# Performance work log

Measured on AMD Instinct MI355X. Metric: run time of the kernel, lower is better.

The kernel has to match this reference:

```python
import jax, jax.numpy as jnp
import numpy as np

N_NODES = 100000


def gcn_conv(x, src, dst, W, b, n_nodes):
    """PyG GCNConv: add self-loops, symmetric deg^-1/2 normalization,
    linear transform, scatter-add aggregation, bias."""
    loop = jnp.arange(n_nodes, dtype=src.dtype)
    s = jnp.concatenate([src, loop])
    d = jnp.concatenate([dst, loop])
    # degree of destination nodes (includes self-loops)
    deg = jax.ops.segment_sum(jnp.ones(s.shape[0], dtype=x.dtype), d,
                              num_segments=n_nodes)
    dis = jnp.where(deg > 0, jax.lax.rsqrt(deg), 0.0)  # deg^-1/2
    norm = dis[s] * dis[d]                              # [E+N]
    h = x @ W                                           # [N, out]
    msg = h[s] * norm[:, None]                          # gather + scale
    out = jax.ops.segment_sum(msg, d, num_segments=n_nodes)  # scatter-add
    return out + b


def setup_inputs() -> dict:
    key = jax.random.key(0)
    k1, k2, k3, k4 = jax.random.split(key, 4)
    F_in, H, C = 500, 64, 10
    x = jax.random.normal(k1, (N_NODES, F_in), dtype=jnp.float32)
    edge_index = jax.random.randint(k2, (2, 1600000), 0, N_NODES,
                                    dtype=jnp.int32)
    W1 = jax.random.normal(k3, (F_in, H), dtype=jnp.float32) / np.sqrt(F_in)
    b1 = jnp.zeros((H,), dtype=jnp.float32)
    W2 = jax.random.normal(k4, (H, C), dtype=jnp.float32) / np.sqrt(H)
    b2 = jnp.zeros((C,), dtype=jnp.float32)
    return {"x": x, "edge_index": edge_index,
            "W1": W1, "b1": b1, "W2": W2, "b2": b2}


def reference(x, edge_index, W1, b1, W2, b2):
    src, dst = edge_index[0], edge_index[1]
    h = gcn_conv(x, src, dst, W1, b1, N_NODES)
    h = jax.nn.relu(h)
    # dropout is identity at inference (training=False)
    out = gcn_conv(h, src, dst, W2, b2, N_NODES)
    return out
```

## Files before the change

### kernel.cpp

```cpp
#include <hip/hip_runtime.h>

#define F_IN 500
#define HDIM 64
#define CDIM 10
#define KPAD 512
#define NSTAGE 16
#define H2LD 16

typedef __attribute__((ext_vector_type(8))) short bf16x8;
typedef __attribute__((ext_vector_type(4))) float floatx4;

__device__ inline unsigned short f2bf(float f) {
    unsigned int u = __float_as_uint(f);
    u += 0x7fffu + ((u >> 16) & 1u);
    return (unsigned short)(u >> 16);
}
__device__ inline float bflo(unsigned int u) { return __uint_as_float(u << 16); }
__device__ inline float bfhi(unsigned int u) { return __uint_as_float(u & 0xffff0000u); }

__device__ inline void split8(float4 a, float4 b, bf16x8& xh, bf16x8& xl) {
    float xv[8] = {a.x, a.y, a.z, a.w, b.x, b.y, b.z, b.w};
#pragma unroll
    for (int j = 0; j < 8; ++j) {
        unsigned int u = __float_as_uint(xv[j]);
        xh[j] = (short)(u >> 16);
        float r = xv[j] - __uint_as_float(u & 0xffff0000u);
        xl[j] = (short)(__float_as_uint(r) >> 16);
    }
}

__global__ __launch_bounds__(256) void prep_kernel(
        const int* __restrict__ dst, int E, int* __restrict__ deg,
        int* __restrict__ erank,
        const float* __restrict__ W1, unsigned short* __restrict__ whf,
        unsigned short* __restrict__ wlf, int degB) {
    int bid = blockIdx.x;
    if (bid < degB) {
        int e = bid * 256 + threadIdx.x;
        if (e < E) erank[e] = atomicAdd(&deg[dst[e]], 1);
    } else {
        int idx = (bid - degB) * 256 + threadIdx.x;
        if (idx >= KPAD * HDIM) return;
        int k = idx >> 6;
        int f = idx & 63;
        float w = (k < F_IN) ? W1[k * HDIM + f] : 0.f;
        unsigned int b = __float_as_uint(w);
        unsigned short hh = (unsigned short)(b >> 16);
        float wl = w - __uint_as_float(b & 0xffff0000u);
        unsigned short ll = (unsigned short)(__float_as_uint(wl) >> 16);
        int kb = k >> 5, q = (k >> 3) & 3, j = k & 7;
        int fb = f >> 4, fl = f & 15;
        int lane = (q << 4) | fl;
        size_t o = ((((size_t)kb * 4 + fb) * 64 + lane) << 3) | (size_t)j;
        whf[o] = hh;
        wlf[o] = ll;
    }
}

__global__ void scan_block_kernel(const int* __restrict__ deg,
                                  int* __restrict__ row_ptr,
                                  int* __restrict__ blk_sum,
                                  float* __restrict__ dis, int Np1) {
    __shared__ int wsum[16];
    int i = blockIdx.x * 1024 + threadIdx.x;
    int v = (i < Np1 - 1) ? deg[i] : 0;
    if (i < Np1 - 1) dis[i] = rsqrtf((float)(v + 1));
    int lane = threadIdx.x & 63;
    int wid = threadIdx.x >> 6;
    int x = v;
#pragma unroll
    for (int off = 1; off < 64; off <<= 1) {
        int y = __shfl_up(x, off);
        if (lane >= off) x += y;
    }
    if (lane == 63) wsum[wid] = x;
    __syncthreads();
    if (threadIdx.x < 16) {
        int ws = wsum[threadIdx.x];
#pragma unroll
        for (int off = 1; off < 16; off <<= 1) {
            int y = __shfl_up(ws, off);
            if ((int)threadIdx.x >= off) ws += y;
        }
        wsum[threadIdx.x] = ws;
    }
    __syncthreads();
    int wp = (wid > 0) ? wsum[wid - 1] : 0;
    if (i < Np1) row_ptr[i] = wp + x - v;
    if (threadIdx.x == 1023) blk_sum[blockIdx.x] = wp + x;
}

__global__ void scan_top_kernel(int* __restrict__ blk_sum, int nb) {
    int carry = 0;
    for (int base = 0; base < nb; base += 64) {
        int i = base + (int)threadIdx.x;
        int v = (i < nb) ? blk_sum[i] : 0;
        int x = v;
#pragma unroll
        for (int off = 1; off < 64; off <<= 1) {
            int y = __shfl_up(x, off);
            if ((int)threadIdx.x >= off) x += y;
        }
        if (i < nb) blk_sum[i] = carry + x - v;
        carry += __shfl(x, 63);
    }
}

__global__ __launch_bounds__(256) void csr_gemm_kernel(
        const float* __restrict__ x, const unsigned short* __restrict__ whf,
        const unsigned short* __restrict__ wlf, const float* __restrict__ dis,
        unsigned short* __restrict__ h1b, int N,
        const int* __restrict__ src, const int* __restrict__ dst,
        const int* __restrict__ erank,
        const int* __restrict__ row_ptr, const int* __restrict__ blk_sum,
        int* __restrict__ csr_src, int E,
        int gemmB) {
    const int bid = blockIdx.x;
    const int g5 = bid / 5;
    const bool isGemm = (bid % 5 == 0) && (g5 < gemmB);
    if (!isGemm) {
        int before = (bid + 4) / 5;
        if (before > gemmB) before = gemmB;
        int cb = bid - before;
        int e = cb * 256 + threadIdx.x;
        if (e >= E) return;
        int d = dst[e];
        csr_src[row_ptr[d] + blk_sum[d >> 10] + erank[e]] = src[e];
        return;
    }
    const int lane = threadIdx.x & 63;
    const int wid = (g5 << 2) + (threadIdx.x >> 6);
    const int n0 = wid * 16;
    if (n0 >= N) return;
    const int q = lane >> 4;
    const int fl = lane & 15;
    const float* xp = x + (size_t)(n0 + fl) * F_IN + q * 8;

    const bf16x8* whv = (const bf16x8*)whf;
    const bf16x8* wlv = (const bf16x8*)wlf;

    floatx4 acc[4];
#pragma unroll
    for (int fb = 0; fb < 4; ++fb) acc[fb] = (floatx4){0.f, 0.f, 0.f, 0.f};

    float4 xa[4], xb[4];
    bf16x8 wh[2][4], wl[2][4];

    xa[0] = *(const float4*)(xp);
    xb[0] = *(const float4*)(xp + 4);
    xa[1] = *(const float4*)(xp + 32);
    xb[1] = *(const float4*)(xp + 36);
    xa[2] = *(const float4*)(xp + 64);
    xb[2] = *(const float4*)(xp + 68);
#pragma unroll
    for (int fb = 0; fb < 4; ++fb) {
        wh[0][fb] = whv[(size_t)fb * 64 + lane];
        wl[0][fb] = wlv[(size_t)fb * 64 + lane];
    }

#pragma unroll
    for (int kb = 0; kb < NSTAGE - 1; ++kb) {
        const int cw = kb & 1, nw = cw ^ 1;
#pragma unroll
        for (int fb = 0; fb < 4; ++fb) {
            wh[nw][fb] = whv[(size_t)((kb + 1) * 4 + fb) * 64 + lane];
            wl[nw][fb] = wlv[(size_t)((kb + 1) * 4 + fb) * 64 + lane];
        }
        if (kb + 3 < NSTAGE - 1) {
            xa[(kb + 3) & 3] = *(const float4*)(xp + (kb + 3) * 32);
            xb[(kb + 3) & 3] = *(const float4*)(xp + (kb + 3) * 32 + 4);
        }
        bf16x8 xh, xl;
        split8(xa[kb & 3], xb[kb & 3], xh, xl);
#pragma unroll
        for (int fb = 0; fb < 4; ++fb) {
            acc[fb] = __builtin_amdgcn_mfma_f32_16x16x32_bf16(xh, wh[cw][fb], acc[fb], 0, 0, 0);
            acc[fb] = __builtin_amdgcn_mfma_f32_16x16x32_bf16(xl, wh[cw][fb], acc[fb], 0, 0, 0);
            acc[fb] = __builtin_amdgcn_mfma_f32_16x16x32_bf16(xh, wl[cw][fb], acc[fb], 0, 0, 0);
        }
    }
    {
        const int kb = NSTAGE - 1;
        float xv[8];
#pragma unroll
        for (int j = 0; j < 8; ++j) {
            int kk = kb * 32 + q * 8 + j;
            xv[j] = (kk < F_IN) ? xp[kb * 32 + j] : 0.f;
        }
        bf16x8 xh, xl;
#pragma unroll
        for (int j = 0; j < 8; ++j) {
            unsigned int u = __float_as_uint(xv[j]);
            xh[j] = (short)(u >> 16);
            float r = xv[j] - __uint_as_float(u & 0xffff0000u);
            xl[j] = (short)(__float_as_uint(r) >> 16);
        }
        const int cw = kb & 1;
#pragma unroll
        for (int fb = 0; fb < 4; ++fb) {
            acc[fb] = __builtin_amdgcn_mfma_f32_16x16x32_bf16(xh, wh[cw][fb], acc[fb], 0, 0, 0);
            acc[fb] = __builtin_amdgcn_mfma_f32_16x16x32_bf16(xl, wh[cw][fb], acc[fb], 0, 0, 0);
            acc[fb] = __builtin_amdgcn_mfma_f32_16x16x32_bf16(xh, wl[cw][fb], acc[fb], 0, 0, 0);
        }
    }
#pragma unroll
    for (int r = 0; r < 4; ++r) {
        int node = n0 + q * 4 + r;
        float dn = dis[node];
#pragma unroll
        for (int fb = 0; fb < 4; ++fb) {
            h1b[(size_t)node * HDIM + fb * 16 + fl] = f2bf(acc[fb][r] * dn);
        }
    }
}

__global__ __launch_bounds__(256) void gather1_l2_kernel(
        const int* __restrict__ row_ptr, const int* __restrict__ blk_sum,
        const int* __restrict__ csr_src, const float* __restrict__ dis,
        const unsigned short* __restrict__ h1b,
        const float* __restrict__ b1, const float* __restrict__ W2,
        float* __restrict__ h2s, int N) {
    __shared__ float sW2[HDIM * CDIM];
    __shared__ float sB1[HDIM];
    for (int i = threadIdx.x; i < HDIM * CDIM; i += 256) sW2[i] = W2[i];
    if (threadIdx.x < HDIM) sB1[threadIdx.x] = b1[threadIdx.x];
    __syncthreads();
    int nid = blockIdx.x * 4 + (threadIdx.x >> 6);
    if (nid >= N) return;
    int node = __builtin_amdgcn_readfirstlane(nid);
    int lane = threadIdx.x & 63;
    int half = lane >> 5;
    int c = lane & 31;
    int beg = row_ptr[node] + blk_sum[node >> 10];
    int end = row_ptr[node + 1] + blk_sum[(node + 1) >> 10];
    float dd = dis[node];
    float a0 = 0.f, a1 = 0.f;
    if (half == 0) {
        unsigned int w = *reinterpret_cast<const unsigned int*>(
            h1b + (size_t)node * HDIM + 2 * c);
        a0 = bflo(w);
        a1 = bfhi(w);
    }
    int p = beg + half;
    for (; p + 14 < end; p += 16) {
        unsigned int wv[8];
#pragma unroll
        for (int i = 0; i < 8; ++i) {
            int s = csr_src[p + 2 * i];
            wv[i] = *reinterpret_cast<const unsigned int*>(
                h1b + (size_t)s * HDIM + 2 * c);
        }
#pragma unroll
        for (int i = 0; i < 8; ++i) {
            a0 += bflo(wv[i]);
            a1 += bfhi(wv[i]);
        }
    }
    for (; p < end; p += 2) {
        int s0 = csr_src[p];
        unsigned int w0 = *reinterpret_cast<const unsigned int*>(
            h1b + (size_t)s0 * HDIM + 2 * c);
        a0 += bflo(w0);
        a1 += bfhi(w0);
    }
    a0 += __shfl_xor(a0, 32);
    a1 += __shfl_xor(a1, 32);
    float t0 = a0 * dd + sB1[2 * c];
    float t1 = a1 * dd + sB1[2 * c + 1];
    t0 = t0 > 0.f ? t0 : 0.f;
    t1 = t1 > 0.f ? t1 : 0.f;
    float pj[CDIM];
#pragma unroll
    for (int j = 0; j < CDIM; ++j)
        pj[j] = t0 * sW2[(2 * c) * CDIM + j] + t1 * sW2[(2 * c + 1) * CDIM + j];
#pragma unroll
    for (int off = 1; off < 32; off <<= 1) {
#pragma unroll
        for (int j = 0; j < CDIM; ++j) pj[j] += __shfl_xor(pj[j], off);
    }
    if (lane < CDIM) {
        float v = pj[0];
#pragma unroll
        for (int j = 1; j < CDIM; ++j)
            if (lane == j) v = pj[j];
        h2s[(size_t)node * H2LD + lane] = v * dd;
    }
}

__global__ __launch_bounds__(256) void gather2_kernel(
        const int* __restrict__ row_ptr, const int* __restrict__ blk_sum,
        const int* __restrict__ csr_src, const float* __restrict__ dis,
        const float* __restrict__ h2s, const float* __restrict__ b2,
        float* __restrict__ out, int N) {
    int nid = blockIdx.x * 4 + (threadIdx.x >> 6);
    if (nid >= N) return;
    int node = __builtin_amdgcn_readfirstlane(nid);
    int lane = threadIdx.x & 63;
    int g = lane >> 4;
    int j = lane & 15;
    int beg = row_ptr[node] + blk_sum[node >> 10];
    int end = row_ptr[node + 1] + blk_sum[(node + 1) >> 10];
    float acc = 0.f;
    int p = beg + g;
    for (; p + 12 < end; p += 16) {
        int s0 = csr_src[p];
        int s1 = csr_src[p + 4];
        int s2 = csr_src[p + 8];
        int s3 = csr_src[p + 12];
        float v0 = (j < CDIM) ? h2s[(size_t)s0 * H2LD + j] : 0.f;
        float v1 = (j < CDIM) ? h2s[(size_t)s1 * H2LD + j] : 0.f;
        float v2 = (j < CDIM) ? h2s[(size_t)s2 * H2LD + j] : 0.f;
        float v3 = (j < CDIM) ? h2s[(size_t)s3 * H2LD + j] : 0.f;
        acc += (v0 + v1) + (v2 + v3);
    }
    for (; p < end; p += 4) {
        int s0 = csr_src[p];
        acc += (j < CDIM) ? h2s[(size_t)s0 * H2LD + j] : 0.f;
    }
    acc += __shfl_xor(acc, 16);
    acc += __shfl_xor(acc, 32);
    if (lane < CDIM) {
        float dd = dis[node];
        out[(size_t)node * CDIM + lane] =
            b2[lane] + dd * (acc + h2s[(size_t)node * H2LD + lane]);
    }
}

static inline char* align256(char* p) {
    return (char*)(((uintptr_t)p + 255) & ~(uintptr_t)255);
}

extern "C" void kernel_launch(void* const* d_in, const int* in_sizes, int n_in,
                              void* d_out, int out_size, void* d_ws,
                              size_t ws_size, hipStream_t stream) {
    const float* x  = (const float*)d_in[0];
    const int*   ei = (const int*)d_in[1];
    const float* W1 = (const float*)d_in[2];
    const float* b1 = (const float*)d_in[3];
    const float* W2 = (const float*)d_in[4];
    const float* b2 = (const float*)d_in[5];

    const int N = in_sizes[0] / F_IN;
    const int E = in_sizes[1] / 2;
    const int* src = ei;
    const int* dst = ei + E;
    float* out = (float*)d_out;

    const int Np1 = N + 1;
    const int nscan_blocks = (Np1 + 1023) / 1024;

    char* w = (char*)d_ws;
    int* deg = (int*)w;                  w = align256(w + (size_t)N * 4);
    char* zero_end = w;
    int* erank = (int*)w;                w = align256(w + (size_t)E * 4);
    float* dis = (float*)w;              w = align256(w + (size_t)N * 4);
    int* row_ptr = (int*)w;              w = align256(w + (size_t)(N + 4) * 4);
    int* blk_sum = (int*)w;              w = align256(w + (size_t)nscan_blocks * 4);
    int* csr_src = (int*)w;              w = align256(w + (size_t)E * 4);
    unsigned short* whf = (unsigned short*)w;  w = align256(w + (size_t)KPAD * HDIM * 2);
    unsigned short* wlf = (unsigned short*)w;  w = align256(w + (size_t)KPAD * HDIM * 2);
    unsigned short* h1b = (unsigned short*)w;  w = align256(w + (size_t)N * HDIM * 2);
    float* h2s = (float*)w;              w = align256(w + (size_t)N * H2LD * 4);

    hipMemsetAsync(deg, 0, (size_t)(zero_end - (char*)deg), stream);

    const int degB = (E + 255) / 256;
    const int wprepB = (KPAD * HDIM + 255) / 256;
    prep_kernel<<<degB + wprepB, 256, 0, stream>>>(dst, E, deg, erank, W1, whf,
                                                   wlf, degB);
    scan_block_kernel<<<nscan_blocks, 1024, 0, stream>>>(deg, row_ptr, blk_sum,
                                                         dis, Np1);
    scan_top_kernel<<<1, 64, 0, stream>>>(blk_sum, nscan_blocks);
    {
        int gemmB = ((N + 15) / 16 + 3) / 4;
        int csrB = (E + 255) / 256;
        csr_gemm_kernel<<<gemmB + csrB, 256, 0, stream>>>(
            x, whf, wlf, dis, h1b, N,
            src, dst, erank, row_ptr, blk_sum, csr_src, E, gemmB);
    }
    gather1_l2_kernel<<<(N + 3) / 4, 256, 0, stream>>>(row_ptr, blk_sum,
                                                       csr_src, dis, h1b,
                                                       b1, W2, h2s, N);
    gather2_kernel<<<(N + 3) / 4, 256, 0, stream>>>(row_ptr, blk_sum, csr_src,
                                                    dis, h2s, b2, out, N);
}
```

Measured before the change: 587.1 us.

## Stage GEMM x and W tiles through LDS with async global-to-LDS double buffering

Rewrites the layer-1 GEMM portion of the fused CSR/GEMM kernel so that x and the split bf16 weights are loaded with global_load_lds into double-buffered, XOR-swizzled shared memory. Each block now computes 128 nodes, with each wave handling two 16-row tiles, instead of 64 nodes loaded directly into registers. The goal is to share weight loads across waves, coalesce the x reads, and overlap the next stage's loads with MFMA work. The cost is 48KB of LDS per block, which also applies to the CSR-fill blocks in the same launch and may lower occupancy. A __syncthreads per K step is also added, and the GEMM/CSR block interleave ratio changes from 1:4 to 1:8.

```diff
diff --git a/kernel.cpp b/kernel.cpp
--- a/kernel.cpp
+++ b/kernel.cpp
@@ -6,6 +6,7 @@
 #define KPAD 512
 #define NSTAGE 16
 #define H2LD 16
+#define BUFSZ 24576
 
 typedef __attribute__((ext_vector_type(8))) short bf16x8;
 typedef __attribute__((ext_vector_type(4))) float floatx4;
@@ -17,6 +18,12 @@
 }
 __device__ inline float bflo(unsigned int u) { return __uint_as_float(u << 16); }
 __device__ inline float bfhi(unsigned int u) { return __uint_as_float(u & 0xffff0000u); }
+
+__device__ inline void gload16(const void* g, void* l) {
+    __builtin_amdgcn_global_load_lds(
+        (const __attribute__((address_space(1))) void*)g,
+        (__attribute__((address_space(3))) void*)l, 16, 0, 0);
+}
 
 __device__ inline void split8(float4 a, float4 b, bf16x8& xh, bf16x8& xl) {
     float xv[8] = {a.x, a.y, a.z, a.w, b.x, b.y, b.z, b.w};
@@ -115,11 +122,13 @@
         const int* __restrict__ row_ptr, const int* __restrict__ blk_sum,
         int* __restrict__ csr_src, int E,
         int gemmB) {
+    __shared__ float4 shmem[2 * BUFSZ / 16];
+    char* sh = (char*)shmem;
     const int bid = blockIdx.x;
-    const int g5 = bid / 5;
-    const bool isGemm = (bid % 5 == 0) && (g5 < gemmB);
+    const int g9 = bid / 9;
+    const bool isGemm = (bid % 9 == 0) && (g9 < gemmB);
     if (!isGemm) {
-        int before = (bid + 4) / 5;
+        int before = (bid + 8) / 9;
         if (before > gemmB) before = gemmB;
         int cb = bid - before;
         int e = cb * 256 + threadIdx.x;
@@ -129,87 +138,81 @@
         return;
     }
     const int lane = threadIdx.x & 63;
-    const int wid = (g5 << 2) + (threadIdx.x >> 6);
-    const int n0 = wid * 16;
-    if (n0 >= N) return;
+    const int w = threadIdx.x >> 6;
+    const int n0 = g9 * 128;
     const int q = lane >> 4;
     const int fl = lane & 15;
-    const float* xp = x + (size_t)(n0 + fl) * F_IN + q * 8;
-
-    const bf16x8* whv = (const bf16x8*)whf;
-    const bf16x8* wlv = (const bf16x8*)wlf;
-
-    floatx4 acc[4];
-#pragma unroll
-    for (int fb = 0; fb < 4; ++fb) acc[fb] = (floatx4){0.f, 0.f, 0.f, 0.f};
-
-    float4 xa[4], xb[4];
-    bf16x8 wh[2][4], wl[2][4];
-
-    xa[0] = *(const float4*)(xp);
-    xb[0] = *(const float4*)(xp + 4);
-    xa[1] = *(const float4*)(xp + 32);
-    xb[1] = *(const float4*)(xp + 36);
-    xa[2] = *(const float4*)(xp + 64);
-    xb[2] = *(const float4*)(xp + 68);
-#pragma unroll
-    for (int fb = 0; fb < 4; ++fb) {
-        wh[0][fb] = whv[(size_t)fb * 64 + lane];
-        wl[0][fb] = wlv[(size_t)fb * 64 + lane];
-    }
-
-#pragma unroll
-    for (int kb = 0; kb < NSTAGE - 1; ++kb) {
-        const int cw = kb & 1, nw = cw ^ 1;
+
+    floatx4 acc[2][4];
+#pragma unroll
+    for (int t = 0; t < 2; ++t)
+#pragma unroll
+        for (int fb = 0; fb < 4; ++fb) acc[t][fb] = (floatx4){0.f, 0.f, 0.f, 0.f};
+
+    auto STAGE = [&](int buf, int kb) {
+        const size_t bb = (size_t)buf * BUFSZ;
+#pragma unroll
+        for (int r2 = 0; r2 < 4; ++r2) {
+            int c = w * 4 + r2;
+            int o = c * 1024 + lane * 16;
+            int ro = o >> 7;
+            int gl = ((o >> 4) & 7) ^ (ro & 7);
+            if (kb == NSTAGE - 1 && gl > 4) gl = 0;
+            int xrow = n0 + ro;
+            if (xrow >= N) xrow = N - 1;
+            gload16(x + (size_t)xrow * F_IN + kb * 32 + gl * 4,
+                    sh + bb + c * 1024);
+        }
+        gload16((const char*)whf + (size_t)kb * 4096 + w * 1024 + lane * 16,
+                sh + bb + 16384 + w * 1024);
+        gload16((const char*)wlf + (size_t)kb * 4096 + w * 1024 + lane * 16,
+                sh + bb + 20480 + w * 1024);
+    };
+
+    STAGE(0, 0);
+    __syncthreads();
+    int cur = 0;
+#pragma unroll
+    for (int kb = 0; kb < NSTAGE; ++kb) {
+        if (kb + 1 < NSTAGE) STAGE(cur ^ 1, kb + 1);
+        const size_t bb = (size_t)cur * BUFSZ;
+        bf16x8 bh[4], bl[4];
 #pragma unroll
         for (int fb = 0; fb < 4; ++fb) {
-            wh[nw][fb] = whv[(size_t)((kb + 1) * 4 + fb) * 64 + lane];
-            wl[nw][fb] = wlv[(size_t)((kb + 1) * 4 + fb) * 64 + lane];
-        }
-        if (kb + 3 < NSTAGE - 1) {
-            xa[(kb + 3) & 3] = *(const float4*)(xp + (kb + 3) * 32);
-            xb[(kb + 3) & 3] = *(const float4*)(xp + (kb + 3) * 32 + 4);
-        }
-        bf16x8 xh, xl;
-        split8(xa[kb & 3], xb[kb & 3], xh, xl);
-#pragma unroll
-        for (int fb = 0; fb < 4; ++fb) {
-            acc[fb] = __builtin_amdgcn_mfma_f32_16x16x32_bf16(xh, wh[cw][fb], acc[fb], 0, 0, 0);
-            acc[fb] = __builtin_amdgcn_mfma_f32_16x16x32_bf16(xl, wh[cw][fb], acc[fb], 0, 0, 0);
-            acc[fb] = __builtin_amdgcn_mfma_f32_16x16x32_bf16(xh, wl[cw][fb], acc[fb], 0, 0, 0);
-        }
-    }
-    {
-        const int kb = NSTAGE - 1;
-        float xv[8];
-#pragma unroll
-        for (int j = 0; j < 8; ++j) {
-            int kk = kb * 32 + q * 8 + j;
-            xv[j] = (kk < F_IN) ? xp[kb * 32 + j] : 0.f;
-        }
-        bf16x8 xh, xl;
-#pragma unroll
-        for (int j = 0; j < 8; ++j) {
-            unsigned int u = __float_as_uint(xv[j]);
-            xh[j] = (short)(u >> 16);
-            float r = xv[j] - __uint_as_float(u & 0xffff0000u);
-            xl[j] = (short)(__float_as_uint(r) >> 16);
-        }
-        const int cw = kb & 1;
-#pragma unroll
-        for (int fb = 0; fb < 4; ++fb) {
-            acc[fb] = __builtin_amdgcn_mfma_f32_16x16x32_bf16(xh, wh[cw][fb], acc[fb], 0, 0, 0);
-            acc[fb] = __builtin_amdgcn_mfma_f32_16x16x32_bf16(xl, wh[cw][fb], acc[fb], 0, 0, 0);
-            acc[fb] = __builtin_amdgcn_mfma_f32_16x16x32_bf16(xh, wl[cw][fb], acc[fb], 0, 0, 0);
-        }
-    }
-#pragma unroll
-    for (int r = 0; r < 4; ++r) {
-        int node = n0 + q * 4 + r;
-        float dn = dis[node];
-#pragma unroll
-        for (int fb = 0; fb < 4; ++fb) {
-            h1b[(size_t)node * HDIM + fb * 16 + fl] = f2bf(acc[fb][r] * dn);
+            bh[fb] = *(const bf16x8*)(sh + bb + 16384 + fb * 1024 + lane * 16);
+            bl[fb] = *(const bf16x8*)(sh + bb + 20480 + fb * 1024 + lane * 16);
+        }
+#pragma unroll
+        for (int t = 0; t < 2; ++t) {
+            int tr = w * 32 + t * 16 + fl;
+            int sw = tr & 7;
+            float4 a0 = *(const float4*)(sh + bb + tr * 128 + (((2 * q) ^ sw) << 4));
+            float4 a1 = *(const float4*)(sh + bb + tr * 128 + (((2 * q + 1) ^ sw) << 4));
+            bf16x8 xh, xl;
+            split8(a0, a1, xh, xl);
+#pragma unroll
+            for (int fb = 0; fb < 4; ++fb) {
+                acc[t][fb] = __builtin_amdgcn_mfma_f32_16x16x32_bf16(xh, bh[fb], acc[t][fb], 0, 0, 0);
+                acc[t][fb] = __builtin_amdgcn_mfma_f32_16x16x32_bf16(xl, bh[fb], acc[t][fb], 0, 0, 0);
+                acc[t][fb] = __builtin_amdgcn_mfma_f32_16x16x32_bf16(xh, bl[fb], acc[t][fb], 0, 0, 0);
+            }
+        }
+        __syncthreads();
+        cur ^= 1;
+    }
+#pragma unroll
+    for (int t = 0; t < 2; ++t) {
+#pragma unroll
+        for (int r = 0; r < 4; ++r) {
+            int node = n0 + w * 32 + t * 16 + q * 4 + r;
+            if (node < N) {
+                float dn = dis[node];
+#pragma unroll
+                for (int fb = 0; fb < 4; ++fb) {
+                    h1b[(size_t)node * HDIM + fb * 16 + fl] =
+                        f2bf(acc[t][fb][r] * dn);
+                }
+            }
         }
     }
 }
@@ -372,7 +375,7 @@
                                                          dis, Np1);
     scan_top_kernel<<<1, 64, 0, stream>>>(blk_sum, nscan_blocks);
     {
-        int gemmB = ((N + 15) / 16 + 3) / 4;
+        int gemmB = (N + 127) / 128;
         int csrB = (E + 255) / 256;
         csr_gemm_kernel<<<gemmB + csrB, 256, 0, stream>>>(
             x, whf, wlf, dis, h1b, N,
```

New measurement: 533.5 us. -9.1%, faster.
